# Kernel tuning notes

Measured on AMD Instinct MI355X. Metric: run time of the kernel, lower is better.

## Reference

```python
import jax, jax.numpy as jnp
import numpy as np

B, S, D, H, DK, FF, NQ = 4, 1024, 512, 64, 8, 2048, 8


def _layernorm(x, w, b, eps=1e-5):
    m = x.mean(-1, keepdims=True)
    v = ((x - m) ** 2).mean(-1, keepdims=True)
    return (x - m) / jnp.sqrt(v + eps) * w + b


def setup_inputs() -> dict:
    key = jax.random.key(0)
    ks = jax.random.split(key, 24)
    std = 0.02
    inp = {
        "x": jax.random.normal(ks[0], (B, S, D), dtype=jnp.float32),
        "Wq": jax.random.normal(ks[1], (D, D)) * std,
        "bq": jnp.zeros((D,)),
        "Wk": jax.random.normal(ks[2], (D, D)) * std,
        "bk": jnp.zeros((D,)),
        "Wv": jax.random.normal(ks[3], (D, D)) * std,
        "bv": jnp.zeros((D,)),
        "theta_attn": jax.random.normal(ks[4], (DK,)) * 0.1,  # trainable RX angles
        "gate_attn": jnp.asarray(1.0, dtype=jnp.float32),
        "Wo": jax.random.normal(ks[5], (D, D)) * std,
        "bo": jnp.zeros((D,)),
        "ln1_w": jnp.ones((D,)),
        "ln1_b": jnp.zeros((D,)),
        "W1": jax.random.normal(ks[6], (FF, NQ)) * std,
        "b1": jnp.zeros((FF,)),
        "W2": jax.random.normal(ks[7], (D, FF)) * std,
        "b2": jnp.zeros((D,)),
        "phi_ffn": jax.random.normal(ks[8], (NQ,)) * 0.1,  # trainable RY angles
        "gate_ffn": jnp.asarray(1.0, dtype=jnp.float32),
        "ln2_w": jnp.ones((D,)),
        "ln2_b": jnp.zeros((D,)),
    }
    return inp


def _attention(x, Wq, bq, Wk, bk, Wv, bv, theta, gate, Wo, bo):
    q = x @ Wq.T + bq
    k = x @ Wk.T + bk
    v = x @ Wv.T + bv
    sep = lambda t: t.reshape(B, S, H, DK).transpose(0, 2, 1, 3)  # [B,H,S,DK]
    qh, kh, vh = sep(q), sep(k), sep(v)
    scores = jnp.einsum("bhsd,bhtd->bhst", qh, kh) / np.sqrt(DK)
    probs = jax.nn.softmax(scores, axis=-1)
    classical = jnp.einsum("bhst,bhtd->bhsd", probs, vh)
    classical = classical.transpose(0, 2, 1, 3).reshape(B, S, D)
    # Quantum head: RX(x_i) then RX(theta_i) -> RX(x_i+theta_i), CNOT ring, <Z_j>.
    # Analytic expectations: <Z_0> = prod_{k=1..DK-1} cos(a_k);
    #                        <Z_j> = prod_{k=0..j}    cos(a_k)   (j >= 1).
    cos_a = jnp.cos(qh + theta)  # [B,H,S,DK]
    cp = jnp.cumprod(cos_a, axis=-1)
    z0 = jnp.prod(cos_a[..., 1:], axis=-1, keepdims=True)
    quantum = jnp.concatenate([z0, cp[..., 1:]], axis=-1)  # [B,H,S,DK]
    quantum = quantum.transpose(0, 2, 1, 3).reshape(B, S, D)
    out = gate * quantum + (1.0 - gate) * classical
    return out @ Wo.T + bo


def _ffn(x, W1, b1, W2, b2, phi, gate):
    xs = x[..., :NQ]  # encoder uses first NQ features
    # Quantum: RX(x_i) then RY(phi_i), measure <Z_i> = cos(x_i)*cos(phi_i).
    qm = jnp.cos(xs) * jnp.cos(phi)
    quantum = jax.nn.relu(qm @ W1.T + b1) @ W2.T + b2
    classical = jax.nn.relu(xs @ W1.T + b1) @ W2.T + b2
    return gate * quantum + (1.0 - gate) * classical


def reference(x, Wq, bq, Wk, bk, Wv, bv, theta_attn, gate_attn, Wo, bo,
              ln1_w, ln1_b, W1, b1, W2, b2, phi_ffn, gate_ffn, ln2_w, ln2_b):
    attn_out = _attention(x, Wq, bq, Wk, bk, Wv, bv, theta_attn, gate_attn, Wo, bo)
    x1 = _layernorm(x + attn_out, ln1_w, ln1_b)
    ffn_out = _ffn(x1, W1, b1, W2, b2, phi_ffn, gate_ffn)
    return _layernorm(x1 + ffn_out, ln2_w, ln2_b)
```

## Files before the change

kernel.cpp:

```cpp
#include <hip/hip_runtime.h>
#include <hip/hip_bf16.h>


typedef short short8 __attribute__((ext_vector_type(8)));
typedef float floatx4 __attribute__((ext_vector_type(4)));

__device__ __forceinline__ unsigned short f2bf_bits(float f) {
  __hip_bfloat16 h = __float2bfloat16(f);
  return *reinterpret_cast<unsigned short*>(&h);
}
__device__ __forceinline__ float bfbits2f(unsigned short u) {
  union { unsigned int u; float f; } c;
  c.u = (unsigned int)u << 16;
  return c.f;
}

#define GLOBAL_LOAD_LDS16(g, l)                                               \
  __builtin_amdgcn_global_load_lds(                                           \
      (const __attribute__((address_space(1))) void*)(g),                     \
      (__attribute__((address_space(3))) void*)(l), 16, 0, 0)

#define WAIT_VMCNT0()   asm volatile("s_waitcnt vmcnt(0)" ::: "memory")
#define WAIT_VMCNT8()   asm volatile("s_waitcnt vmcnt(8)" ::: "memory")
#define WAIT_VMCNT10()  asm volatile("s_waitcnt vmcnt(10)" ::: "memory")
#define WAIT_VMCNT16()  asm volatile("s_waitcnt vmcnt(16)" ::: "memory")
#define WAIT_LGKM0()    asm volatile("s_waitcnt lgkmcnt(0)" ::: "memory")
#define BARRIER()       __builtin_amdgcn_s_barrier()
#define CFENCE()        asm volatile("" ::: "memory")

__device__ __forceinline__ void gemm_core_ks(
    const __hip_bfloat16* __restrict__ A,
    const __hip_bfloat16* __restrict__ W,
    int K, int kbeg, int ntiles, long m0, long n0, int lane,
    __hip_bfloat16* sh, floatx4 acc[4][4])
{
  const int srow = lane >> 3;
  const int gchunk = (lane & 7) ^ srow;
  const int frow = lane & 15;
  const int fk = lane >> 4;

  auto stage = [&](int kt, __hip_bfloat16* buf) {
#pragma unroll
    for (int ib = 0; ib < 8; ++ib) {
      const int row = ib * 8 + srow;
      GLOBAL_LOAD_LDS16(A + (m0 + row) * K + kt + gchunk * 8, buf + ib * 512);
      GLOBAL_LOAD_LDS16(W + (n0 + row) * K + kt + gchunk * 8, buf + 4096 + ib * 512);
    }
  };

  WAIT_LGKM0();
  stage(kbeg, sh);
  if (ntiles > 1) stage(kbeg + 64, sh + 8192);

  for (int t = 0; t < ntiles; ++t) {
    __hip_bfloat16* buf = sh + (t & 1) * 8192;
    if (t < ntiles - 1) { WAIT_VMCNT16(); }
    else               { WAIT_VMCNT0(); }

    short8 af[2][4], bf[2][4];
#pragma unroll
    for (int ks = 0; ks < 2; ++ks)
#pragma unroll
      for (int i = 0; i < 4; ++i) {
        const int ar = i * 16 + frow;
        af[ks][i] = *(const short8*)(buf + ar * 64 + (((ks * 4 + fk) ^ (ar & 7)) << 3));
        bf[ks][i] = *(const short8*)(buf + 4096 + ar * 64 + (((ks * 4 + fk) ^ (ar & 7)) << 3));
      }
    WAIT_LGKM0();
    if (t + 2 < ntiles) stage(kbeg + ((t + 2) << 6), buf);
#pragma unroll
    for (int ks = 0; ks < 2; ++ks)
#pragma unroll
      for (int i = 0; i < 4; ++i)
#pragma unroll
        for (int j = 0; j < 4; ++j)
          acc[i][j] = __builtin_amdgcn_mfma_f32_16x16x32_bf16(
              af[ks][i], bf[ks][j], acc[i][j], 0, 0, 0);
  }
}

__device__ __forceinline__ bool ks_reduce(
    floatx4 acc[4][4], __hip_bfloat16* sh, int wid, int lane)
{
  float* red = (float*)(sh + 16384);
  if (wid == 1) {
#pragma unroll
    for (int i = 0; i < 4; ++i)
#pragma unroll
      for (int j = 0; j < 4; ++j)
        *(floatx4*)(red + ((i * 4 + j) * 64 + lane) * 4) = acc[i][j];
    WAIT_LGKM0();
  }
  CFENCE(); BARRIER(); CFENCE();
  if (wid == 1) return false;
#pragma unroll
  for (int i = 0; i < 4; ++i)
#pragma unroll
    for (int j = 0; j < 4; ++j)
      acc[i][j] += *(const floatx4*)(red + ((i * 4 + j) * 64 + lane) * 4);
  return true;
}

__device__ __forceinline__ void store_f32(
    floatx4 acc[4][4], float* __restrict__ C, const float* __restrict__ bias,
    long m0, long n0, int lane)
{
  const int col_l = lane & 15;
  const int row_l = (lane >> 4) << 2;
#pragma unroll
  for (int j = 0; j < 4; ++j) {
    const long col = n0 + j * 16 + col_l;
    const float bv = bias[col];
#pragma unroll
    for (int i = 0; i < 4; ++i)
#pragma unroll
      for (int r = 0; r < 4; ++r)
        C[(m0 + i * 16 + row_l + r) * 512 + col] = acc[i][j][r] + bv;
  }
}

__device__ __forceinline__ void store_bf16(
    floatx4 acc[4][4], __hip_bfloat16* __restrict__ C,
    const float* __restrict__ bias, long m0, long n0, int lane)
{
  const int col_l = lane & 15;
  const int row_l = (lane >> 4) << 2;
#pragma unroll
  for (int j = 0; j < 4; ++j) {
    const long col = n0 + j * 16 + col_l;
    const float bv = bias[col];
#pragma unroll
    for (int i = 0; i < 4; ++i)
#pragma unroll
      for (int r = 0; r < 4; ++r)
        C[(m0 + i * 16 + row_l + r) * 512 + col] =
            __float2bfloat16(acc[i][j][r] + bv);
  }
}

__global__ __launch_bounds__(128) void gemm_qkv(
    const __hip_bfloat16* __restrict__ x_bf,
    const __hip_bfloat16* __restrict__ Wq,
    const __hip_bfloat16* __restrict__ Wk,
    const __hip_bfloat16* __restrict__ Wv,
    const float* __restrict__ bq, const float* __restrict__ bk,
    const float* __restrict__ bvv,
    __hip_bfloat16* __restrict__ mix,
    float* __restrict__ Qb, float* __restrict__ Kb, float* __restrict__ Vb,
    const float* __restrict__ theta, const float* __restrict__ gateA)
{
  const int z = blockIdx.z;
  const float g = *gateA;
  if (z > 0 && g == 1.0f) return;
  const __hip_bfloat16* W = (z == 0) ? Wq : (z == 1) ? Wk : Wv;
  const float* bias = (z == 0) ? bq : (z == 1) ? bk : bvv;
  float* Cf = (z == 0) ? Qb : (z == 1) ? Kb : Vb;

  __shared__ __align__(16) __hip_bfloat16 sh[32768];
  const int tid = threadIdx.x;
  const int wid = tid >> 6;
  const int lane = tid & 63;
  const long m0 = (long)blockIdx.x * 64;
  const long n0 = (long)blockIdx.y * 64;
  floatx4 acc[4][4];
#pragma unroll
  for (int i = 0; i < 4; ++i)
#pragma unroll
    for (int j = 0; j < 4; ++j) acc[i][j] = (floatx4){0.f, 0.f, 0.f, 0.f};

  gemm_core_ks(x_bf, W, 512, wid * 256, 4, m0, n0, lane, sh + wid * 16384, acc);
  if (!ks_reduce(acc, sh, wid, lane)) return;

  const int col_l = lane & 15;
  const int row_l = (lane >> 4) << 2;

  if (z > 0 || g != 1.0f) store_f32(acc, Cf, bias, m0, n0, lane);
  if (z == 0) {
    float* shf = (float*)sh;
    WAIT_LGKM0();
#pragma unroll
    for (int j = 0; j < 4; ++j) {
      const long col = n0 + j * 16 + col_l;
      const float bv = bias[col];
#pragma unroll
      for (int i = 0; i < 4; ++i)
#pragma unroll
        for (int r = 0; r < 4; ++r)
          shf[(i * 16 + row_l + r) * 64 + j * 16 + col_l] = acc[i][j][r] + bv;
    }
    WAIT_LGKM0();
    float th[8];
#pragma unroll
    for (int i = 0; i < 8; ++i) th[i] = theta[i];
#pragma unroll
    for (int t = 0; t < 8; ++t) {
      const int gidx = t * 64 + lane;
      const int row = gidx >> 3;
      const int hh = gidx & 7;
      const float* src = shf + row * 64 + hh * 8;
      float c[8];
#pragma unroll
      for (int i = 0; i < 8; ++i) c[i] = __cosf(src[i] + th[i]);
      float o[8];
      float p = c[1];
#pragma unroll
      for (int i = 2; i < 8; ++i) p *= c[i];
      o[0] = p;
      float cp = c[0];
#pragma unroll
      for (int i = 1; i < 8; ++i) { cp *= c[i]; o[i] = cp; }
      union { unsigned short u16[8]; uint4 v; } pk;
#pragma unroll
      for (int i = 0; i < 8; ++i) pk.u16[i] = f2bf_bits(o[i]);
      *(uint4*)(mix + (m0 + row) * 512 + n0 + hh * 8) = pk.v;
    }
  }
}

__global__ __launch_bounds__(512) void wo_lnffn(
    const __hip_bfloat16* __restrict__ A,
    const __hip_bfloat16* __restrict__ W,
    const float* __restrict__ bo,
    const float* __restrict__ x,
    const float* __restrict__ lw, const float* __restrict__ lb,
    float* __restrict__ x1, const float* __restrict__ phi,
    const float* __restrict__ W1,
    const float* __restrict__ b1,
    __hip_bfloat16* __restrict__ hq, __hip_bfloat16* __restrict__ hc,
    const float* __restrict__ gateF)
{
  __shared__ __align__(16) __hip_bfloat16 sh[68608];
  const int tid = threadIdx.x;
  const int wid = tid >> 6;
  const int lane = tid & 63;
  const long m0 = (long)blockIdx.x * 16;
  const long n0w = (long)wid * 64;

  const int srow = lane >> 3;
  const int gchunk = (lane & 7) ^ srow;
  const int frow = lane & 15;
  const int fk = lane >> 4;

  __hip_bfloat16* shA = sh;
  __hip_bfloat16* shW = sh + 3072 + wid * 8192;

  auto stageA = [&](int kt, int slot) {
    __hip_bfloat16* buf = shA + slot * 1024;
#pragma unroll
    for (int i = 0; i < 2; ++i) {
      const int row = i * 8 + srow;
      GLOBAL_LOAD_LDS16(A + (m0 + row) * 512 + kt + gchunk * 8, buf + i * 512);
    }
  };
  auto stageW = [&](int kt, int slot) {
    __hip_bfloat16* buf = shW + slot * 4096;
#pragma unroll
    for (int i = 0; i < 8; ++i) {
      const int row = i * 8 + srow;
      GLOBAL_LOAD_LDS16(W + (n0w + row) * 512 + kt + gchunk * 8, buf + i * 512);
    }
  };

  floatx4 acc[4];
#pragma unroll
  for (int j = 0; j < 4; ++j) acc[j] = (floatx4){0.f, 0.f, 0.f, 0.f};

  if (wid == 0) stageA(0, 0);
  stageW(0, 0);
  if (wid == 0) stageA(64, 1);
  stageW(64, 1);

  for (int t = 0; t < 8; ++t) {
    const int wslot = t & 1;
    const int aslot = t % 3;
    if (t < 7) { if (wid == 0) WAIT_VMCNT10(); else WAIT_VMCNT8(); }
    else       { WAIT_VMCNT0(); }
    BARRIER();

    short8 af[2], bf[2][4];
#pragma unroll
    for (int ks = 0; ks < 2; ++ks) {
      af[ks] = *(const short8*)(shA + aslot * 1024 + frow * 64 +
                                (((ks * 4 + fk) ^ (frow & 7)) << 3));
#pragma unroll
      for (int j = 0; j < 4; ++j) {
        const int wr = j * 16 + frow;
        bf[ks][j] = *(const short8*)(shW + wslot * 4096 + wr * 64 +
                                     (((ks * 4 + fk) ^ (frow & 7)) << 3));
      }
    }
    WAIT_LGKM0();
    if (t < 6) {
      if (wid == 0) stageA((t + 2) << 6, (t + 2) % 3);
      stageW((t + 2) << 6, wslot);
    }
#pragma unroll
    for (int ks = 0; ks < 2; ++ks)
#pragma unroll
      for (int j = 0; j < 4; ++j)
        acc[j] = __builtin_amdgcn_mfma_f32_16x16x32_bf16(
            af[ks], bf[ks][j], acc[j], 0, 0, 0);
  }

  BARRIER();

  float* attnL = (float*)sh;
  float* qmL = attnL + 16 * 516;
  float* xsL = qmL + 128;
  {
    const int col_l = lane & 15;
    const int row_l = (lane >> 4) << 2;
#pragma unroll
    for (int j = 0; j < 4; ++j) {
      const int c = (int)n0w + j * 16 + col_l;
      const float bv = bo[c];
#pragma unroll
      for (int r = 0; r < 4; ++r)
        attnL[(row_l + r) * 516 + c] = acc[j][r] + bv;
    }
  }
  WAIT_LGKM0();
  BARRIER();

  const int rr = tid >> 5;
  const int cl = tid & 31;
  const long rowg = m0 + rr;
  float sv[16];
  float sum = 0.f, ssq = 0.f;
#pragma unroll
  for (int i = 0; i < 16; ++i) {
    const int c = cl + i * 32;
    const float v = x[rowg * 512 + c] + attnL[rr * 516 + c];
    sv[i] = v; sum += v; ssq += v * v;
  }
#pragma unroll
  for (int off = 16; off > 0; off >>= 1) {
    sum += __shfl_xor(sum, off, 32);
    ssq += __shfl_xor(ssq, off, 32);
  }
  const float mean = sum * (1.0f / 512.0f);
  const float var = ssq * (1.0f / 512.0f) - mean * mean;
  const float rstd = rsqrtf(fmaxf(var, 0.0f) + 1e-5f);
#pragma unroll
  for (int i = 0; i < 16; ++i) {
    const int c = cl + i * 32;
    const float o = (sv[i] - mean) * rstd * lw[c] + lb[c];
    x1[rowg * 512 + c] = o;
    if (i == 0 && cl < 8) {
      qmL[rr * 8 + cl] = __cosf(o) * __cosf(phi[cl]);
      xsL[rr * 8 + cl] = o;
    }
  }
  WAIT_LGKM0();
  BARRIER();

  const int n4 = tid << 2;
  float w1r[4][8];
#pragma unroll
  for (int jr = 0; jr < 4; ++jr) {
    float4 wa = *(const float4*)(W1 + (long)(n4 + jr) * 8);
    float4 wb = *(const float4*)(W1 + (long)(n4 + jr) * 8 + 4);
    w1r[jr][0] = wa.x; w1r[jr][1] = wa.y; w1r[jr][2] = wa.z; w1r[jr][3] = wa.w;
    w1r[jr][4] = wb.x; w1r[jr][5] = wb.y; w1r[jr][6] = wb.z; w1r[jr][7] = wb.w;
  }
  float4 bb = *(const float4*)(b1 + n4);
  const float b1a[4] = {bb.x, bb.y, bb.z, bb.w};
  const float gv = *gateF;
#pragma unroll 2
  for (int r = 0; r < 16; ++r) {
    float qm8[8];
#pragma unroll
    for (int k = 0; k < 8; ++k) qm8[k] = qmL[r * 8 + k];
    union { unsigned short u16[4]; ushort4 v; } pk;
#pragma unroll
    for (int jr = 0; jr < 4; ++jr) {
      float a = b1a[jr];
#pragma unroll
      for (int k = 0; k < 8; ++k) a += qm8[k] * w1r[jr][k];
      pk.u16[jr] = f2bf_bits(fmaxf(a, 0.0f));
    }
    *(ushort4*)(hq + (m0 + r) * 2048 + n4) = pk.v;
    if (gv != 1.0f) {
      float xs8[8];
#pragma unroll
      for (int k = 0; k < 8; ++k) xs8[k] = xsL[r * 8 + k];
#pragma unroll
      for (int jr = 0; jr < 4; ++jr) {
        float a = b1a[jr];
#pragma unroll
        for (int k = 0; k < 8; ++k) a += xs8[k] * w1r[jr][k];
        pk.u16[jr] = f2bf_bits(fmaxf(a, 0.0f));
      }
      *(ushort4*)(hc + (m0 + r) * 2048 + n4) = pk.v;
    }
  }
}

__global__ __launch_bounds__(128) void gemm_ffnout(
    const __hip_bfloat16* __restrict__ hq,
    const __hip_bfloat16* __restrict__ hc,
    const __hip_bfloat16* __restrict__ W2, const float* __restrict__ b2,
    __hip_bfloat16* __restrict__ Fb, __hip_bfloat16* __restrict__ Fc,
    const float* __restrict__ gateF)
{
  const int z = blockIdx.z;
  if (z == 1 && *gateF == 1.0f) return;
  const __hip_bfloat16* A = z ? hc : hq;
  __hip_bfloat16* C = z ? Fc : Fb;
  __shared__ __align__(16) __hip_bfloat16 sh[32768];
  const int tid = threadIdx.x;
  const int wid = tid >> 6;
  const int lane = tid & 63;
  const long m0 = (long)blockIdx.x * 64;
  const long n0 = (long)blockIdx.y * 64;
  floatx4 acc[4][4];
#pragma unroll
  for (int i = 0; i < 4; ++i)
#pragma unroll
    for (int j = 0; j < 4; ++j) acc[i][j] = (floatx4){0.f, 0.f, 0.f, 0.f};
  gemm_core_ks(A, W2, 2048, wid * 1024, 16, m0, n0, lane, sh + wid * 16384, acc);
  if (!ks_reduce(acc, sh, wid, lane)) return;
  store_bf16(acc, C, b2, m0, n0, lane);
}

__device__ __forceinline__ void cvt_one(const float* s, __hip_bfloat16* d, int n,
                                        long tid, long stride) {
  const int n4 = n >> 2;
  for (long i = tid; i < n4; i += stride) {
    float4 v = ((const float4*)s)[i];
    ushort4 u;
    u.x = f2bf_bits(v.x); u.y = f2bf_bits(v.y);
    u.z = f2bf_bits(v.z); u.w = f2bf_bits(v.w);
    ((ushort4*)d)[i] = u;
  }
}

__global__ __launch_bounds__(256) void prep_inputs(
    const float* x, __hip_bfloat16* x_bf,
    const float* Wq, __hip_bfloat16* Wq_bf,
    const float* Wo, __hip_bfloat16* Wo_bf,
    const float* W2, __hip_bfloat16* W2_bf,
    const float* Wk, __hip_bfloat16* Wk_bf,
    const float* Wv, __hip_bfloat16* Wv_bf,
    const float* gateA)
{
  const long stride = (long)gridDim.x * blockDim.x;
  const long tid = (long)blockIdx.x * blockDim.x + threadIdx.x;
  cvt_one(x, x_bf, 4096 * 512, tid, stride);
  cvt_one(Wq, Wq_bf, 512 * 512, tid, stride);
  cvt_one(Wo, Wo_bf, 512 * 512, tid, stride);
  cvt_one(W2, W2_bf, 512 * 2048, tid, stride);
  if (*gateA != 1.0f) {
    cvt_one(Wk, Wk_bf, 512 * 512, tid, stride);
    cvt_one(Wv, Wv_bf, 512 * 512, tid, stride);
  }
}

__global__ __launch_bounds__(256) void attn_blend(
    const float* __restrict__ Qb, const float* __restrict__ Kb,
    const float* __restrict__ Vb, __hip_bfloat16* __restrict__ mix,
    const float* __restrict__ gateA)
{
  const float g = *gateA;
  if (g == 1.0f) return;
  const int idx = blockIdx.x * blockDim.x + threadIdx.x;
  if (idx >= 4 * 64 * 1024) return;
  const int s = idx & 1023;
  const int h = (idx >> 10) & 63;
  const int b = idx >> 16;
  const long qoff = ((long)(b * 1024 + s)) * 512 + h * 8;
  float q[8];
#pragma unroll
  for (int i = 0; i < 8; ++i) q[i] = Qb[qoff + i] * 0.35355339059327373f;
  float m = -INFINITY, l = 0.0f, acc[8];
#pragma unroll
  for (int i = 0; i < 8; ++i) acc[i] = 0.0f;
  for (int t = 0; t < 1024; ++t) {
    const long koff = ((long)(b * 1024 + t)) * 512 + h * 8;
    const float* kr = Kb + koff;
    const float* vr = Vb + koff;
    float sc = 0.0f;
#pragma unroll
    for (int i = 0; i < 8; ++i) sc += q[i] * kr[i];
    float nm = fmaxf(m, sc);
    float corr = __expf(m - nm);
    float p = __expf(sc - nm);
    l = l * corr + p;
#pragma unroll
    for (int i = 0; i < 8; ++i) acc[i] = acc[i] * corr + p * vr[i];
    m = nm;
  }
  const float inv = 1.0f / l;
  union { unsigned short u16[8]; uint4 v; } pk;
  pk.v = *(const uint4*)(mix + qoff);
#pragma unroll
  for (int i = 0; i < 8; ++i) {
    float quant = bfbits2f(pk.u16[i]);
    pk.u16[i] = f2bf_bits(g * quant + (1.0f - g) * acc[i] * inv);
  }
  *(uint4*)(mix + qoff) = pk.v;
}

__global__ __launch_bounds__(256) void add_ln3(
    const float* __restrict__ x1, const __hip_bfloat16* __restrict__ Fb,
    const __hip_bfloat16* __restrict__ Fc, const float* __restrict__ gateF,
    const float* __restrict__ lw, const float* __restrict__ lb,
    float* __restrict__ out)
{
  const int tid = threadIdx.x;
  const int wv = tid >> 6, lane = tid & 63;
  const int row = blockIdx.x * 4 + wv;
  const long base = (long)row * 512;
  const int c0 = lane * 8;
  float4 a0 = *(const float4*)(x1 + base + c0);
  float4 a1 = *(const float4*)(x1 + base + c0 + 4);
  union { unsigned short u16[8]; uint4 v; } fb;
  fb.v = *(const uint4*)(Fb + base + c0);
  const float xa[8] = {a0.x, a0.y, a0.z, a0.w, a1.x, a1.y, a1.z, a1.w};
  float s[8];
  const float gv = *gateF;
  if (gv != 1.0f) {
    union { unsigned short u16[8]; uint4 v; } fc;
    fc.v = *(const uint4*)(Fc + base + c0);
    const float om = 1.0f - gv;
#pragma unroll
    for (int i = 0; i < 8; ++i)
      s[i] = xa[i] + gv * bfbits2f(fb.u16[i]) + om * bfbits2f(fc.u16[i]);
  } else {
#pragma unroll
    for (int i = 0; i < 8; ++i) s[i] = xa[i] + bfbits2f(fb.u16[i]);
  }
  float sum = 0.f, ssq = 0.f;
#pragma unroll
  for (int i = 0; i < 8; ++i) { sum += s[i]; ssq += s[i] * s[i]; }
#pragma unroll
  for (int off = 32; off > 0; off >>= 1) {
    sum += __shfl_xor(sum, off);
    ssq += __shfl_xor(ssq, off);
  }
  const float mean = sum * (1.0f / 512.0f);
  const float var = ssq * (1.0f / 512.0f) - mean * mean;
  const float rstd = rsqrtf(fmaxf(var, 0.0f) + 1e-5f);
  float4 w0 = *(const float4*)(lw + c0);
  float4 w1 = *(const float4*)(lw + c0 + 4);
  float4 g0 = *(const float4*)(lb + c0);
  float4 g1 = *(const float4*)(lb + c0 + 4);
  const float wf[8] = {w0.x, w0.y, w0.z, w0.w, w1.x, w1.y, w1.z, w1.w};
  const float gf8[8] = {g0.x, g0.y, g0.z, g0.w, g1.x, g1.y, g1.z, g1.w};
  float o[8];
#pragma unroll
  for (int i = 0; i < 8; ++i) o[i] = (s[i] - mean) * rstd * wf[i] + gf8[i];
  *(float4*)(out + base + c0) = (float4){o[0], o[1], o[2], o[3]};
  *(float4*)(out + base + c0 + 4) = (float4){o[4], o[5], o[6], o[7]};
}

extern "C" void kernel_launch(void* const* d_in, const int* in_sizes, int n_in,
                              void* d_out, int out_size, void* d_ws, size_t ws_size,
                              hipStream_t stream) {
  const float* x     = (const float*)d_in[0];
  const float* Wq    = (const float*)d_in[1];
  const float* bq    = (const float*)d_in[2];
  const float* Wk    = (const float*)d_in[3];
  const float* bk    = (const float*)d_in[4];
  const float* Wv    = (const float*)d_in[5];
  const float* bv    = (const float*)d_in[6];
  const float* theta = (const float*)d_in[7];
  const float* gateA = (const float*)d_in[8];
  const float* Wo    = (const float*)d_in[9];
  const float* bo    = (const float*)d_in[10];
  const float* ln1w  = (const float*)d_in[11];
  const float* ln1b  = (const float*)d_in[12];
  const float* W1    = (const float*)d_in[13];
  const float* b1    = (const float*)d_in[14];
  const float* W2    = (const float*)d_in[15];
  const float* b2    = (const float*)d_in[16];
  const float* phi   = (const float*)d_in[17];
  const float* gateF = (const float*)d_in[18];
  const float* ln2w  = (const float*)d_in[19];
  const float* ln2b  = (const float*)d_in[20];
  float* out = (float*)d_out;

  const size_t MB = 1024 * 1024;
  char* wsb = (char*)d_ws;
  __hip_bfloat16* x_bf    = (__hip_bfloat16*)(wsb + 0 * MB);
  __hip_bfloat16* Wq_bf   = (__hip_bfloat16*)(wsb + 4 * MB);
  __hip_bfloat16* Wo_bf   = (__hip_bfloat16*)(wsb + 4 * MB + 512 * 1024);
  __hip_bfloat16* W2_bf   = (__hip_bfloat16*)(wsb + 5 * MB);
  __hip_bfloat16* mix_bf  = (__hip_bfloat16*)(wsb + 8 * MB);
  float*          x1      = (float*)(wsb + 16 * MB);
  __hip_bfloat16* hq_bf   = (__hip_bfloat16*)(wsb + 24 * MB);
  __hip_bfloat16* Fb_bf   = (__hip_bfloat16*)(wsb + 40 * MB);
  float*          Qb      = (float*)(wsb + 52 * MB);
  __hip_bfloat16* Wk_bf   = (__hip_bfloat16*)(wsb + 60 * MB);
  __hip_bfloat16* Wv_bf   = (__hip_bfloat16*)(wsb + 60 * MB + 512 * 1024);
  float*          Kb2     = (float*)(wsb + 61 * MB);
  float*          Vb2     = (float*)(wsb + 69 * MB);
  __hip_bfloat16* hc_bf   = (__hip_bfloat16*)(wsb + 77 * MB);
  __hip_bfloat16* Fc_bf   = (__hip_bfloat16*)(wsb + 93 * MB);

  prep_inputs<<<1024, 256, 0, stream>>>(
      x, x_bf, Wq, Wq_bf, Wo, Wo_bf, W2, W2_bf, Wk, Wk_bf, Wv, Wv_bf, gateA);
  gemm_qkv<<<dim3(64, 8, 3), 128, 0, stream>>>(
      x_bf, Wq_bf, Wk_bf, Wv_bf, bq, bk, bv,
      mix_bf, Qb, Kb2, Vb2, theta, gateA);
  attn_blend<<<1024, 256, 0, stream>>>(Qb, Kb2, Vb2, mix_bf, gateA);
  wo_lnffn<<<256, 512, 0, stream>>>(
      mix_bf, Wo_bf, bo, x, ln1w, ln1b, x1, phi, W1, b1, hq_bf, hc_bf, gateF);
  gemm_ffnout<<<dim3(64, 8, 2), 128, 0, stream>>>(
      hq_bf, hc_bf, W2_bf, b2, Fb_bf, Fc_bf, gateF);
  add_ln3<<<1024, 256, 0, stream>>>(x1, Fb_bf, Fc_bf, gateF, ln2w, ln2b, out);
}
```

Before: 146.3 us.

## Retile QKV GEMM to 32x32 single-wave blocks without split-K

Replaces the 64x64 split-K GEMM (two waves, each doing half the K range, then an LDS reduction) with a 32x32 tile per single-wave block that walks the full K in a double-buffered global-to-LDS pipeline. The grid grows from 512 to 2048 blocks for the Q projection, which spreads work across more CUs and removes the cross-wave reduction and its barrier. The quantum-head epilogue is reindexed for the smaller tile. A swizzle index elsewhere changes from frow to wr, which gives the same value because j*16 does not affect the low three bits. In exchange, the smaller tiles reuse each staged operand less, so more global loads are issued per FLOP.

```diff
diff --git a/kernel.cpp b/kernel.cpp
--- a/kernel.cpp
+++ b/kernel.cpp
@@ -101,9 +101,9 @@
   return true;
 }
 
-__device__ __forceinline__ void store_f32(
-    floatx4 acc[4][4], float* __restrict__ C, const float* __restrict__ bias,
-    long m0, long n0, int lane)
+__device__ __forceinline__ void store_bf16(
+    floatx4 acc[4][4], __hip_bfloat16* __restrict__ C,
+    const float* __restrict__ bias, long m0, long n0, int lane)
 {
   const int col_l = lane & 15;
   const int row_l = (lane >> 4) << 2;
@@ -115,30 +115,12 @@
     for (int i = 0; i < 4; ++i)
 #pragma unroll
       for (int r = 0; r < 4; ++r)
-        C[(m0 + i * 16 + row_l + r) * 512 + col] = acc[i][j][r] + bv;
-  }
-}
-
-__device__ __forceinline__ void store_bf16(
-    floatx4 acc[4][4], __hip_bfloat16* __restrict__ C,
-    const float* __restrict__ bias, long m0, long n0, int lane)
-{
-  const int col_l = lane & 15;
-  const int row_l = (lane >> 4) << 2;
-#pragma unroll
-  for (int j = 0; j < 4; ++j) {
-    const long col = n0 + j * 16 + col_l;
-    const float bv = bias[col];
-#pragma unroll
-    for (int i = 0; i < 4; ++i)
-#pragma unroll
-      for (int r = 0; r < 4; ++r)
         C[(m0 + i * 16 + row_l + r) * 512 + col] =
             __float2bfloat16(acc[i][j][r] + bv);
   }
 }
 
-__global__ __launch_bounds__(128) void gemm_qkv(
+__global__ __launch_bounds__(64) void gemm_qkv(
     const __hip_bfloat16* __restrict__ x_bf,
     const __hip_bfloat16* __restrict__ Wq,
     const __hip_bfloat16* __restrict__ Wk,
@@ -156,48 +138,102 @@
   const float* bias = (z == 0) ? bq : (z == 1) ? bk : bvv;
   float* Cf = (z == 0) ? Qb : (z == 1) ? Kb : Vb;
 
-  __shared__ __align__(16) __hip_bfloat16 sh[32768];
-  const int tid = threadIdx.x;
-  const int wid = tid >> 6;
-  const int lane = tid & 63;
-  const long m0 = (long)blockIdx.x * 64;
-  const long n0 = (long)blockIdx.y * 64;
-  floatx4 acc[4][4];
-#pragma unroll
-  for (int i = 0; i < 4; ++i)
-#pragma unroll
-    for (int j = 0; j < 4; ++j) acc[i][j] = (floatx4){0.f, 0.f, 0.f, 0.f};
-
-  gemm_core_ks(x_bf, W, 512, wid * 256, 4, m0, n0, lane, sh + wid * 16384, acc);
-  if (!ks_reduce(acc, sh, wid, lane)) return;
+  __shared__ __align__(16) __hip_bfloat16 sh[8192];
+  const int lane = threadIdx.x;
+  const long n0 = (long)blockIdx.x * 32;
+  const long m0 = (long)blockIdx.y * 32;
+  const int srow = lane >> 3;
+  const int gchunk = (lane & 7) ^ srow;
+  const int frow = lane & 15;
+  const int fk = lane >> 4;
+
+  auto stage = [&](int kt, int slot) {
+    __hip_bfloat16* buf = sh + slot * 4096;
+#pragma unroll
+    for (int ib = 0; ib < 4; ++ib) {
+      const int row = ib * 8 + srow;
+      GLOBAL_LOAD_LDS16(x_bf + (m0 + row) * 512 + kt + gchunk * 8,
+                        buf + ib * 512);
+      GLOBAL_LOAD_LDS16(W + (n0 + row) * 512 + kt + gchunk * 8,
+                        buf + 2048 + ib * 512);
+    }
+  };
+
+  floatx4 acc[2][2];
+#pragma unroll
+  for (int i = 0; i < 2; ++i)
+#pragma unroll
+    for (int j = 0; j < 2; ++j) acc[i][j] = (floatx4){0.f, 0.f, 0.f, 0.f};
+
+  stage(0, 0);
+  stage(64, 1);
+
+  for (int t = 0; t < 8; ++t) {
+    __hip_bfloat16* buf = sh + (t & 1) * 4096;
+    if (t < 7) { WAIT_VMCNT8(); }
+    else       { WAIT_VMCNT0(); }
+
+    short8 af[2][2], bf[2][2];
+#pragma unroll
+    for (int ks = 0; ks < 2; ++ks)
+#pragma unroll
+      for (int i = 0; i < 2; ++i) {
+        const int ar = i * 16 + frow;
+        af[ks][i] = *(const short8*)(buf + ar * 64 +
+                                     (((ks * 4 + fk) ^ (ar & 7)) << 3));
+        bf[ks][i] = *(const short8*)(buf + 2048 + ar * 64 +
+                                     (((ks * 4 + fk) ^ (ar & 7)) << 3));
+      }
+    WAIT_LGKM0();
+    if (t + 2 < 8) stage((t + 2) << 6, t & 1);
+#pragma unroll
+    for (int ks = 0; ks < 2; ++ks)
+#pragma unroll
+      for (int i = 0; i < 2; ++i)
+#pragma unroll
+        for (int j = 0; j < 2; ++j)
+          acc[i][j] = __builtin_amdgcn_mfma_f32_16x16x32_bf16(
+              af[ks][i], bf[ks][j], acc[i][j], 0, 0, 0);
+  }
 
   const int col_l = lane & 15;
   const int row_l = (lane >> 4) << 2;
 
-  if (z > 0 || g != 1.0f) store_f32(acc, Cf, bias, m0, n0, lane);
+  if (z > 0 || g != 1.0f) {
+#pragma unroll
+    for (int j = 0; j < 2; ++j) {
+      const long col = n0 + j * 16 + col_l;
+      const float bv = bias[col];
+#pragma unroll
+      for (int i = 0; i < 2; ++i)
+#pragma unroll
+        for (int r = 0; r < 4; ++r)
+          Cf[(m0 + i * 16 + row_l + r) * 512 + col] = acc[i][j][r] + bv;
+    }
+  }
   if (z == 0) {
     float* shf = (float*)sh;
     WAIT_LGKM0();
 #pragma unroll
-    for (int j = 0; j < 4; ++j) {
-      const long col = n0 + j * 16 + col_l;
-      const float bv = bias[col];
-#pragma unroll
-      for (int i = 0; i < 4; ++i)
+    for (int j = 0; j < 2; ++j) {
+      const int c = j * 16 + col_l;
+      const float bv = bias[n0 + c];
+#pragma unroll
+      for (int i = 0; i < 2; ++i)
 #pragma unroll
         for (int r = 0; r < 4; ++r)
-          shf[(i * 16 + row_l + r) * 64 + j * 16 + col_l] = acc[i][j][r] + bv;
+          shf[(i * 16 + row_l + r) * 32 + c] = acc[i][j][r] + bv;
     }
     WAIT_LGKM0();
     float th[8];
 #pragma unroll
     for (int i = 0; i < 8; ++i) th[i] = theta[i];
 #pragma unroll
-    for (int t = 0; t < 8; ++t) {
-      const int gidx = t * 64 + lane;
-      const int row = gidx >> 3;
-      const int hh = gidx & 7;
-      const float* src = shf + row * 64 + hh * 8;
+    for (int q = 0; q < 2; ++q) {
+      const int gidx = q * 64 + lane;
+      const int row = gidx >> 2;
+      const int hh = gidx & 3;
+      const float* src = shf + row * 32 + hh * 8;
       float c[8];
 #pragma unroll
       for (int i = 0; i < 8; ++i) c[i] = __cosf(src[i] + th[i]);
@@ -286,7 +322,7 @@
       for (int j = 0; j < 4; ++j) {
         const int wr = j * 16 + frow;
         bf[ks][j] = *(const short8*)(shW + wslot * 4096 + wr * 64 +
-                                     (((ks * 4 + fk) ^ (frow & 7)) << 3));
+                                     (((ks * 4 + fk) ^ (wr & 7)) << 3));
       }
     }
     WAIT_LGKM0();
@@ -600,7 +636,7 @@
 
   prep_inputs<<<1024, 256, 0, stream>>>(
       x, x_bf, Wq, Wq_bf, Wo, Wo_bf, W2, W2_bf, Wk, Wk_bf, Wv, Wv_bf, gateA);
-  gemm_qkv<<<dim3(64, 8, 3), 128, 0, stream>>>(
+  gemm_qkv<<<dim3(16, 128, 3), 64, 0, stream>>>(
       x_bf, Wq_bf, Wk_bf, Wv_bf, bq, bk, bv,
       mix_bf, Qb, Kb2, Vb2, theta, gateA);
   attn_blend<<<1024, 256, 0, stream>>>(Qb, Kb2, Vb2, mix_bf, gateA);
```

Result: no change. 148.7 us (+1.6%).
